# Kernel optimization log

Measured on AMD Instinct MI355X. Metric: run time of the kernel, lower is better.

## Reference

```python
import jax, jax.numpy as jnp
import numpy as np


def _edt(fg):
    """Exact 2D Euclidean distance transform.

    fg: [B, H, W] bool, True = foreground. Returns, for every pixel, the
    Euclidean distance to the nearest background (False) pixel; 0 on
    background pixels. Matches scipy.ndimage.distance_transform_edt.
    Two-pass separable algorithm: exact 1D city-block distance along axis 1,
    then exact lower-envelope min along axis 2 via a scan over columns.
    """
    B, H, W = fg.shape
    BIG = jnp.float32(H + W)  # larger than any achievable distance
    bg = ~fg
    row_idx = jnp.arange(H, dtype=jnp.float32)[None, :, None]  # [1,H,1]

    def dist_to_prev_bg(bg_mask):
        # distance (along axis 1) to the most recent background pixel above
        last = jax.lax.cummax(jnp.where(bg_mask, row_idx, -BIG), axis=1)
        return row_idx - last

    d_up = dist_to_prev_bg(bg)
    d_down = jnp.flip(dist_to_prev_bg(jnp.flip(bg, axis=1)), axis=1)
    g = jnp.minimum(jnp.minimum(d_up, d_down), BIG)  # [B,H,W] 1D vertical dist
    g2 = g * g

    # Second pass: D2[b,h,x] = min_{x'} g2[b,h,x'] + (x - x')^2  (exact EDT^2)
    x = jnp.arange(W, dtype=jnp.float32)  # [W]

    def body(D2, inp):
        xp, g2col = inp  # scalar, [B,H]
        cand = g2col[:, :, None] + (x - xp) ** 2  # [B,H,W]
        return jnp.minimum(D2, cand), None

    D2_init = jnp.full((B, H, W), (2.0 * BIG) ** 2, dtype=jnp.float32)
    D2, _ = jax.lax.scan(body, D2_init, (x, jnp.moveaxis(g2, 2, 0)))
    return jnp.sqrt(D2)


def setup_inputs() -> dict:
    key = jax.random.key(0)
    k1, k2 = jax.random.split(key)
    B, C, H, W = 8, 4, 256, 256
    logits = jax.random.normal(k1, (B, C, H, W), dtype=jnp.float32)
    pred_softmax = jax.nn.softmax(logits, axis=1)
    mask = jax.random.randint(k2, (B, H, W), 0, C, dtype=jnp.int64)
    return {"pred_softmax": pred_softmax, "mask": mask}


def reference(pred_softmax, mask):
    B, C, H, W = pred_softmax.shape
    norm = np.float32(np.sqrt(H * H + W * W) + 1e-6)
    loss = jnp.float32(0.0)
    for c in range(1, C):  # small fixed number of classes
        fg = mask == c
        dist = _edt(fg) / norm  # [B,H,W]; all-zeros when class absent, as in ref
        loss = loss + jnp.mean(pred_softmax[:, c] * dist)
    return loss / max(C - 1, 1)
```

## Files before the change

kernel.cpp:

```cpp
#include <hip/hip_runtime.h>
#include <math.h>

#define B_    8
#define C_    4
#define H_    256
#define W_    256
#define NCLS  3
#define NROWS (NCLS * B_ * H_)
#define BIGVAL (1 << 26)

__global__ __launch_bounds__(256) void vert_g_kernel(const int* __restrict__ mask,
                                                     unsigned short* __restrict__ gbuf) {
    const int lane = threadIdx.x & 63;
    const int hc   = threadIdx.x >> 6;
    const int blk  = blockIdx.x;
    const int wt   = blk & 3;
    const int b    = (blk >> 2) & 7;
    const int c_i  = blk >> 5;
    const int cls  = c_i + 1;
    const int w    = (wt << 6) + lane;

    __shared__ int last_sh[4][64];
    __shared__ int first_sh[4][64];

    const int* mptr = mask + (b << 16) + (hc << 14) + w;
    unsigned long long bg = 0ull;
    #pragma unroll 8
    for (int i = 0; i < 64; ++i) {
        int m = mptr[i << 8];
        bg |= (unsigned long long)(m != cls) << i;
    }
    last_sh[hc][lane]  = bg ? ((hc << 6) + 63 - __builtin_clzll(bg)) : -512;
    first_sh[hc][lane] = bg ? ((hc << 6) + __builtin_ctzll(bg)) : (1 << 20);
    __syncthreads();

    int carry_up = -512;
    #pragma unroll
    for (int k = 0; k < 4; ++k)
        if (k < hc) carry_up = max(carry_up, last_sh[k][lane]);
    int carry_dn = 1 << 20;
    #pragma unroll
    for (int k = 0; k < 4; ++k)
        if (k > hc) carry_dn = min(carry_dn, first_sh[k][lane]);

    unsigned short* gout = gbuf + (((c_i << 3) + b) << 16) + (hc << 14) + w;
    #pragma unroll 4
    for (int i = 0; i < 64; ++i) {
        int h = (hc << 6) + i;
        unsigned long long le = bg & (~0ull >> (63 - i));
        int last = le ? ((hc << 6) + 63 - __builtin_clzll(le)) : carry_up;
        int du = h - last;
        unsigned long long ge = bg >> i;
        int first = ge ? (h + __builtin_ctzll(ge)) : carry_dn;
        int dd = first - h;
        int g = min(min(du, dd), 512);
        gout[i << 8] = (unsigned short)g;
    }
}

__global__ __launch_bounds__(256) void horiz_kernel(const unsigned short* __restrict__ gbuf,
                                                    const float* __restrict__ pred,
                                                    double* __restrict__ acc) {
    const int lane = threadIdx.x & 63;
    const int wv   = threadIdx.x >> 6;
    const int row  = blockIdx.x * 4 + wv;
    const int c_i  = row >> 11;
    const int b    = (row >> 8) & 7;
    const int h    = row & 255;
    const int cls  = c_i + 1;

    __shared__ __align__(16) int ext[4][512];
    __shared__ double wsum[4];

    const int x0 = lane << 2;
    ushort4 gv = *(const ushort4*)(gbuf + row * 256 + x0);
    int g0 = gv.x, g1 = gv.y, g2v = gv.z, g3 = gv.w;
    int q0 = g0 * g0, q1 = g1 * g1, q2 = g2v * g2v, q3 = g3 * g3;
    *(int4*)&ext[wv][128 + x0] = make_int4(q0, q1, q2, q3);
    ext[wv][lane]       = BIGVAL;
    ext[wv][64 + lane]  = BIGVAL;
    ext[wv][384 + lane] = BIGVAL;
    ext[wv][448 + lane] = BIGVAL;
    __syncthreads();

    int gm = max(max(g0, g1), max(g2v, g3));
    #pragma unroll
    for (int off = 32; off > 0; off >>= 1) gm = max(gm, __shfl_xor(gm, off, 64));
    const int R = gm - 1;

    int D2[4] = { q0, q1, q2, q3 };
    const int* e = &ext[wv][128];

    if (R >= 120) {
        for (int xp = 0; xp < 256; ++xp) {
            int s = e[xp];
            #pragma unroll
            for (int j = 0; j < 4; ++j) {
                int d = (x0 + j) - xp;
                int cand = s + d * d;
                D2[j] = (cand < D2[j]) ? cand : D2[j];
            }
        }
    } else if (R >= 1) {
        for (int o = 1; o <= R; ++o) {
            int oo = o * o;
            #pragma unroll
            for (int j = 0; j < 4; ++j) {
                int xj = x0 + j;
                int c1 = e[xj + o];
                int c2 = e[xj - o];
                int cm = (c1 < c2) ? c1 : c2;
                int cand = cm + oo;
                D2[j] = (cand < D2[j]) ? cand : D2[j];
            }
        }
    }

    const float* prow = pred + ((((b << 2) + cls) << 8) + h) * 256;
    float4 pv = *(const float4*)(prow + x0);
    double sum = sqrt((double)D2[0]) * (double)pv.x
               + sqrt((double)D2[1]) * (double)pv.y
               + sqrt((double)D2[2]) * (double)pv.z
               + sqrt((double)D2[3]) * (double)pv.w;
    #pragma unroll
    for (int off = 32; off > 0; off >>= 1) sum += __shfl_xor(sum, off, 64);
    if (lane == 0) wsum[wv] = sum;
    __syncthreads();
    if (threadIdx.x == 0)
        acc[blockIdx.x] = wsum[0] + wsum[1] + wsum[2] + wsum[3];
}

__global__ __launch_bounds__(64) void final_kernel(const double* __restrict__ acc,
                                                   float* __restrict__ out) {
    int lane = threadIdx.x;
    double s = 0.0;
    for (int i = lane; i < NROWS / 4; i += 64) s += acc[i];
    #pragma unroll
    for (int off = 32; off > 0; off >>= 1) s += __shfl_xor(s, off, 64);
    if (lane == 0) {
        double nd = sqrt(131072.0) + 1e-6;
        double norm = (double)(float)nd;
        out[0] = (float)(s / norm / ((double)NCLS * (double)(B_ * H_ * W_)));
    }
}

extern "C" void kernel_launch(void* const* d_in, const int* in_sizes, int n_in,
                              void* d_out, int out_size, void* d_ws, size_t ws_size,
                              hipStream_t stream) {
    const float* pred = (const float*)d_in[0];
    const int*   mask = (const int*)d_in[1];
    float* out = (float*)d_out;

    char* ws = (char*)d_ws;
    double* acc = (double*)ws;
    unsigned short* gbuf = (unsigned short*)(ws + 16384);

    vert_g_kernel<<<NCLS * 8 * 4, 256, 0, stream>>>(mask, gbuf);
    horiz_kernel<<<NROWS / 4, 256, 0, stream>>>(gbuf, pred, acc);
    final_kernel<<<1, 64, 0, stream>>>(acc, out);
}
```

Measured before the change: 76.13 us.

## Batch mask loads, hoist pred load, drop barriers, use fp32 sqrt

The vertical pass now issues all 64 strided mask loads up front into registers before building the background bitmask, so more loads are in flight in this low-occupancy kernel. The horizontal pass loads the pred row early to overlap it with the envelope loop, and drops both __syncthreads because each wave only touches its own LDS row and writes its own per-row partial sum. Double-precision sqrt becomes fp32 sqrtf, and the final reduction uses 256 threads over the larger per-row accumulator array. The risks are higher register pressure from the 64-element array, reliance on wave-synchronous LDS ordering, and small rounding differences from fp32 sqrt.

```diff
diff --git a/kernel.cpp b/kernel.cpp
--- a/kernel.cpp
+++ b/kernel.cpp
@@ -24,12 +24,14 @@
     __shared__ int first_sh[4][64];
 
     const int* mptr = mask + (b << 16) + (hc << 14) + w;
+    int m[64];
+    #pragma unroll
+    for (int i = 0; i < 64; ++i) m[i] = mptr[i << 8];
     unsigned long long bg = 0ull;
-    #pragma unroll 8
-    for (int i = 0; i < 64; ++i) {
-        int m = mptr[i << 8];
-        bg |= (unsigned long long)(m != cls) << i;
-    }
+    #pragma unroll
+    for (int i = 0; i < 64; ++i)
+        bg |= (unsigned long long)(m[i] != cls) << i;
+
     last_sh[hc][lane]  = bg ? ((hc << 6) + 63 - __builtin_clzll(bg)) : -512;
     first_sh[hc][lane] = bg ? ((hc << 6) + __builtin_ctzll(bg)) : (1 << 20);
     __syncthreads();
@@ -70,10 +72,12 @@
     const int cls  = c_i + 1;
 
     __shared__ __align__(16) int ext[4][512];
-    __shared__ double wsum[4];
 
     const int x0 = lane << 2;
+    const float* prow = pred + ((((b << 2) + cls) << 8) + h) * 256;
+    float4 pv = *(const float4*)(prow + x0);
     ushort4 gv = *(const ushort4*)(gbuf + row * 256 + x0);
+
     int g0 = gv.x, g1 = gv.y, g2v = gv.z, g3 = gv.w;
     int q0 = g0 * g0, q1 = g1 * g1, q2 = g2v * g2v, q3 = g3 * g3;
     *(int4*)&ext[wv][128 + x0] = make_int4(q0, q1, q2, q3);
@@ -81,7 +85,6 @@
     ext[wv][64 + lane]  = BIGVAL;
     ext[wv][384 + lane] = BIGVAL;
     ext[wv][448 + lane] = BIGVAL;
-    __syncthreads();
 
     int gm = max(max(g0, g1), max(g2v, g3));
     #pragma unroll
@@ -116,31 +119,31 @@
         }
     }
 
-    const float* prow = pred + ((((b << 2) + cls) << 8) + h) * 256;
-    float4 pv = *(const float4*)(prow + x0);
-    double sum = sqrt((double)D2[0]) * (double)pv.x
-               + sqrt((double)D2[1]) * (double)pv.y
-               + sqrt((double)D2[2]) * (double)pv.z
-               + sqrt((double)D2[3]) * (double)pv.w;
+    double sum = (double)(sqrtf((float)D2[0]) * pv.x)
+               + (double)(sqrtf((float)D2[1]) * pv.y)
+               + (double)(sqrtf((float)D2[2]) * pv.z)
+               + (double)(sqrtf((float)D2[3]) * pv.w);
     #pragma unroll
     for (int off = 32; off > 0; off >>= 1) sum += __shfl_xor(sum, off, 64);
-    if (lane == 0) wsum[wv] = sum;
-    __syncthreads();
-    if (threadIdx.x == 0)
-        acc[blockIdx.x] = wsum[0] + wsum[1] + wsum[2] + wsum[3];
+    if (lane == 0) acc[row] = sum;
 }
 
-__global__ __launch_bounds__(64) void final_kernel(const double* __restrict__ acc,
-                                                   float* __restrict__ out) {
-    int lane = threadIdx.x;
+__global__ __launch_bounds__(256) void final_kernel(const double* __restrict__ acc,
+                                                    float* __restrict__ out) {
+    const int t = threadIdx.x;
+    __shared__ double wsum[4];
     double s = 0.0;
-    for (int i = lane; i < NROWS / 4; i += 64) s += acc[i];
+    #pragma unroll
+    for (int i = 0; i < NROWS / 256; ++i) s += acc[t + i * 256];
     #pragma unroll
     for (int off = 32; off > 0; off >>= 1) s += __shfl_xor(s, off, 64);
-    if (lane == 0) {
+    if ((t & 63) == 0) wsum[t >> 6] = s;
+    __syncthreads();
+    if (t == 0) {
+        double total = wsum[0] + wsum[1] + wsum[2] + wsum[3];
         double nd = sqrt(131072.0) + 1e-6;
         double norm = (double)(float)nd;
-        out[0] = (float)(s / norm / ((double)NCLS * (double)(B_ * H_ * W_)));
+        out[0] = (float)(total / norm / ((double)NCLS * (double)(B_ * H_ * W_)));
     }
 }
 
@@ -153,9 +156,9 @@
 
     char* ws = (char*)d_ws;
     double* acc = (double*)ws;
-    unsigned short* gbuf = (unsigned short*)(ws + 16384);
+    unsigned short* gbuf = (unsigned short*)(ws + 65536);
 
     vert_g_kernel<<<NCLS * 8 * 4, 256, 0, stream>>>(mask, gbuf);
     horiz_kernel<<<NROWS / 4, 256, 0, stream>>>(gbuf, pred, acc);
-    final_kernel<<<1, 64, 0, stream>>>(acc, out);
+    final_kernel<<<1, 256, 0, stream>>>(acc, out);
 }
```

Result: faster. 68.31 us (-10.3%).
